# Kernel tuning notes

Hardware: AMD Instinct MI355X
Metric: run time of the kernel (lower is better)

## Reference

```python
import jax, jax.numpy as jnp
import numpy as np
import math

D_K = 1024
HEADS = 16
HEAD_DIM = 64

def setup_inputs() -> dict:
    key = jax.random.key(0)
    ks = jax.random.split(key, 9)
    B, S, E = 2, 2048, D_K
    sc = 0.02
    return {
        "x": jax.random.normal(ks[0], (B, S, E), dtype=jnp.float32),
        "mask": 1,
        "Wq": jax.random.normal(ks[1], (E, E), dtype=jnp.float32) * sc,
        "bq": jnp.zeros((E,), dtype=jnp.float32),
        "Wk": jax.random.normal(ks[2], (E, E), dtype=jnp.float32) * sc,
        "bk": jnp.zeros((E,), dtype=jnp.float32),
        "Wv": jax.random.normal(ks[3], (E, E), dtype=jnp.float32) * sc,
        "bv": jnp.zeros((E,), dtype=jnp.float32),
        "Wo": jax.random.normal(ks[4], (E, E), dtype=jnp.float32) * sc,
        "bo": jnp.zeros((E,), dtype=jnp.float32),
    }

def reference(x, mask, Wq, bq, Wk, bk, Wv, bv, Wo, bo):
    B, S, E = x.shape
    H, Dh = HEADS, HEAD_DIM
    # QKV projections; split heads: [B, H, S, Dh]
    q = (x @ Wq + bq).reshape(B, S, H, Dh).transpose(0, 2, 1, 3)
    k = (x @ Wk + bk).reshape(B, S, H, Dh).transpose(0, 2, 1, 3)
    v = (x @ Wv + bv).reshape(B, S, H, Dh).transpose(0, 2, 1, 3)
    # NOTE: original scales by sqrt(d_k) (full model dim), not sqrt(head_dim)
    scores = jnp.einsum('bhsd,bhtd->bhst', q, k) / math.sqrt(E)
    if mask:
        causal = jnp.tril(jnp.ones((S, S), dtype=bool))
        scores = jnp.where(causal[None, None], scores, jnp.float32(-1e9))
    attn = jax.nn.softmax(scores, axis=-1)
    out = jnp.einsum('bhst,bhtd->bhsd', attn, v)  # [B,H,S,Dh]
    out = out.transpose(0, 2, 1, 3).reshape(B, S, E)
    return out @ Wo + bo
```

## Files before the change

### kernel.cpp

```cpp
#include <hip/hip_runtime.h>

#define HEADS  16
#define DH     64
#define SEQ    2048
#define NBATCH 2
#define EMB    1024
#define MTOT   (NBATCH * SEQ)

#define QSCALE 0.045084220027780106f

typedef short  s16x8 __attribute__((ext_vector_type(8)));
typedef float  f32x4 __attribute__((ext_vector_type(4)));
typedef unsigned short u16;
typedef unsigned short u16x4 __attribute__((ext_vector_type(4)));

__device__ __forceinline__ u16 f2bf(float f) {
  unsigned u = __builtin_bit_cast(unsigned, f);
  u += 0x7fffu + ((u >> 16) & 1u);
  return (u16)(u >> 16);
}

__device__ __forceinline__ void gll16(const u16* g, u16* l) {
  __builtin_amdgcn_global_load_lds(
      (const __attribute__((address_space(1))) unsigned int*)g,
      (__attribute__((address_space(3))) unsigned int*)l, 16, 0, 0);
}

__global__ void cvt_x_kernel(const float* __restrict__ x, u16* __restrict__ xb) {
  int i = (blockIdx.x * 256 + threadIdx.x) * 4;
  float4 v = *(const float4*)(x + i);
  u16x4 o;
  o.x = f2bf(v.x); o.y = f2bf(v.y); o.z = f2bf(v.z); o.w = f2bf(v.w);
  *(u16x4*)(xb + i) = o;
}

__global__ __launch_bounds__(256) void cvt_wt_kernel(const float* __restrict__ Wq, const float* __restrict__ Wk,
                                                     const float* __restrict__ Wv, const float* __restrict__ Wo,
                                                     u16* __restrict__ Wqt, u16* __restrict__ Wkt,
                                                     u16* __restrict__ Wvt, u16* __restrict__ Wot) {
  __shared__ float tile[64][65];
  const float* W; u16* T;
  switch (blockIdx.z) {
    case 0:  W = Wq; T = Wqt; break;
    case 1:  W = Wk; T = Wkt; break;
    case 2:  W = Wv; T = Wvt; break;
    default: W = Wo; T = Wot; break;
  }
  const int n0 = blockIdx.x * 64, k0 = blockIdx.y * 64;
  const int tr = threadIdx.x >> 4;
  const int tc = (threadIdx.x & 15) * 4;
#pragma unroll
  for (int rr = 0; rr < 64; rr += 16) {
    float4 v = *(const float4*)&W[(size_t)(k0 + tr + rr) * EMB + n0 + tc];
    tile[tr + rr][tc + 0] = v.x;
    tile[tr + rr][tc + 1] = v.y;
    tile[tr + rr][tc + 2] = v.z;
    tile[tr + rr][tc + 3] = v.w;
  }
  __syncthreads();
#pragma unroll
  for (int rr = 0; rr < 64; rr += 16) {
    u16x4 o;
    o.x = f2bf(tile[tc + 0][tr + rr]);
    o.y = f2bf(tile[tc + 1][tr + rr]);
    o.z = f2bf(tile[tc + 2][tr + rr]);
    o.w = f2bf(tile[tc + 3][tr + rr]);
    *(u16x4*)&T[(size_t)(n0 + tr + rr) * EMB + k0 + tc] = o;
  }
}

__device__ __forceinline__ void gemm_core(const u16* __restrict__ A, const u16* __restrict__ Bt,
                                          u16* As, u16* Bs, int m0, int n0, f32x4 acc[4][2]) {
  const int tid = threadIdx.x;
  const int lane = tid & 63, w = tid >> 6;
  const int wm = w >> 1, wn = w & 1;
  const int lr = lane & 15, lq = lane >> 4;
#pragma unroll
  for (int i = 0; i < 4; i++)
#pragma unroll
    for (int j = 0; j < 2; j++)
      acc[i][j] = (f32x4){0.f, 0.f, 0.f, 0.f};

  for (int k0 = 0; k0 < EMB; k0 += 64) {
    __syncthreads();
#pragma unroll
    for (int j = 0; j < 4; j++) {
      int c = tid + 256 * j;
      int row = c >> 3, c8 = (c & 7) ^ (row & 7);
      gll16(&A[(size_t)(m0 + row) * EMB + k0 + c8 * 8],
            &As[(w * 64 + 256 * j) * 8]);
    }
#pragma unroll
    for (int j = 0; j < 2; j++) {
      int c = tid + 256 * j;
      int row = c >> 3, c8 = (c & 7) ^ (row & 7);
      gll16(&Bt[(size_t)(n0 + row) * EMB + k0 + c8 * 8],
            &Bs[(w * 64 + 256 * j) * 8]);
    }
    __syncthreads();
#pragma unroll
    for (int kk8 = 0; kk8 < 8; kk8 += 4) {
      s16x8 af[4], bf[2];
#pragma unroll
      for (int i = 0; i < 4; i++) {
        int row = wm * 64 + i * 16 + lr;
        af[i] = *(const s16x8*)&As[row * 64 + (((kk8 + lq) ^ (row & 7)) * 8)];
      }
#pragma unroll
      for (int j = 0; j < 2; j++) {
        int row = wn * 32 + j * 16 + lr;
        bf[j] = *(const s16x8*)&Bs[row * 64 + (((kk8 + lq) ^ (row & 7)) * 8)];
      }
#pragma unroll
      for (int i = 0; i < 4; i++)
#pragma unroll
        for (int j = 0; j < 2; j++)
          acc[i][j] = __builtin_amdgcn_mfma_f32_16x16x32_bf16(af[i], bf[j], acc[i][j], 0, 0, 0);
    }
  }
}

__global__ __launch_bounds__(256) void gemm_qkv(const u16* __restrict__ xb,
                                                const u16* __restrict__ Wqt, const u16* __restrict__ Wkt,
                                                const u16* __restrict__ Wvt,
                                                const float* __restrict__ bq, const float* __restrict__ bk,
                                                const float* __restrict__ bv,
                                                u16* __restrict__ Qb, u16* __restrict__ Kb,
                                                u16* __restrict__ Vtb) {
  __shared__ __align__(16) u16 As[128 * 64];
  __shared__ __align__(16) u16 Bs[64 * 64];
  const u16* Bt; const float* bias; u16* out; const int mode = blockIdx.z;
  switch (mode) {
    case 0:  Bt = Wqt; bias = bq; out = Qb;  break;
    case 1:  Bt = Wkt; bias = bk; out = Kb;  break;
    default: Bt = Wvt; bias = bv; out = Vtb; break;
  }
  const int m0 = blockIdx.y * 128, n0 = blockIdx.x * 64;
  f32x4 acc[4][2];
  gemm_core(xb, Bt, As, Bs, m0, n0, acc);

  const int tid = threadIdx.x, lane = tid & 63, w = tid >> 6;
  const int wm = w >> 1, wn = w & 1;
  const int lr = lane & 15, lq = lane >> 4;
#pragma unroll
  for (int i = 0; i < 4; i++) {
#pragma unroll
    for (int j = 0; j < 2; j++) {
      int col   = n0 + wn * 32 + j * 16 + lr;
      int mbase = m0 + wm * 64 + i * 16 + lq * 4;
      float bv_ = bias[col];
      int h = col >> 6, d = col & 63;
      if (mode == 0) {
#pragma unroll
        for (int r = 0; r < 4; r++) {
          int m = mbase + r, b = m >> 11, s = m & (SEQ - 1);
          out[((size_t)(b * HEADS + h) * SEQ + s) * DH + d] = f2bf((acc[i][j][r] + bv_) * QSCALE);
        }
      } else if (mode == 1) {
#pragma unroll
        for (int r = 0; r < 4; r++) {
          int m = mbase + r, b = m >> 11, s = m & (SEQ - 1);
          out[((size_t)(b * HEADS + h) * SEQ + s) * DH + d] = f2bf(acc[i][j][r] + bv_);
        }
      } else {
        int b = mbase >> 11, s = mbase & (SEQ - 1);
        u16x4 pk;
        pk.x = f2bf(acc[i][j][0] + bv_);
        pk.y = f2bf(acc[i][j][1] + bv_);
        pk.z = f2bf(acc[i][j][2] + bv_);
        pk.w = f2bf(acc[i][j][3] + bv_);
        *(u16x4*)&out[((size_t)(b * HEADS + h) * DH + d) * SEQ + s] = pk;
      }
    }
  }
}

__global__ __launch_bounds__(256) void gemm_out(const u16* __restrict__ A, const u16* __restrict__ Bt,
                                                const float* __restrict__ bias, float* __restrict__ out) {
  __shared__ __align__(16) u16 As[128 * 64];
  __shared__ __align__(16) u16 Bs[64 * 64];
  const int m0 = blockIdx.y * 128, n0 = blockIdx.x * 64;
  f32x4 acc[4][2];
  gemm_core(A, Bt, As, Bs, m0, n0, acc);

  const int tid = threadIdx.x, lane = tid & 63, w = tid >> 6;
  const int wm = w >> 1, wn = w & 1;
  const int lr = lane & 15, lq = lane >> 4;
#pragma unroll
  for (int i = 0; i < 4; i++) {
#pragma unroll
    for (int j = 0; j < 2; j++) {
      int col   = n0 + wn * 32 + j * 16 + lr;
      int mbase = m0 + wm * 64 + i * 16 + lq * 4;
      float bv_ = bias[col];
#pragma unroll
      for (int r = 0; r < 4; r++)
        out[(size_t)(mbase + r) * EMB + col] = acc[i][j][r] + bv_;
    }
  }
}

__global__ __launch_bounds__(512, 4) void attn_fwd(const u16* __restrict__ Q,
                                                   const u16* __restrict__ Kg,
                                                   const u16* __restrict__ Vt,
                                                   u16* __restrict__ O) {
  __shared__ __align__(16) u16 smem[33280];
  const int tid = threadIdx.x, lane = tid & 63, w = tid >> 6;
  const int g = w >> 2, wg = w & 3;
  const int lr = lane & 15, lq = lane >> 4;
  const int bh = blockIdx.y, bx = blockIdx.x;
  const int qtA = bx, qtB = 31 - bx;
  const int rowoff = wg * 16;
  u16* Ks = smem + (g ? 11520 : 0);
  u16* Vs = smem + (g ? 16640 : 5120);
  u16* pw = smem + 23040 + w * 1280;
  const size_t qkbase = (size_t)bh * SEQ * DH;
  const size_t vbase  = (size_t)bh * DH * SEQ;
  const u16* kgp = Kg + qkbase;
  const u16* vtp = Vt + vbase;
  const int t256 = tid & 255;
  const int b = bh >> 4, hh = bh & 15;

  {
    int r = t256 >> 4, c = (t256 & 15) * 4;
    u16 one = 0x3F80;
    u16x4 val = (r == 0) ? (u16x4){one, one, one, one} : (u16x4){0, 0, 0, 0};
    *(u16x4*)&Vs[(64 + r) * 80 + c] = val;
  }

  s16x8 qf0, qf1;
  {
    const int myqt0 = g ? qtB : qtA;
    const u16* qp = Q + qkbase + (size_t)(myqt0 * 64 + rowoff + lr) * DH;
    qf0 = *(const s16x8*)&qp[lq * 8];
    qf1 = *(const s16x8*)&qp[32 + lq * 8];
  }
  f32x4 o[4], os;
#pragma unroll
  for (int t = 0; t < 4; t++) o[t] = (f32x4){0.f, 0.f, 0.f, 0.f};
  os = (f32x4){0.f, 0.f, 0.f, 0.f};

  const int srow = t256 >> 3, soff = (t256 & 7) * 8;
  int kt0 = g ? (16 - bx) : 0;
  s16x8 kr0 = *(const s16x8*)&kgp[(size_t)(kt0 * 64 + srow) * DH + soff];
  s16x8 kr1 = *(const s16x8*)&kgp[(size_t)(kt0 * 64 + srow + 32) * DH + soff];
  s16x8 vr0 = *(const s16x8*)&vtp[(size_t)srow * SEQ + kt0 * 64 + soff];
  s16x8 vr1 = *(const s16x8*)&vtp[(size_t)(srow + 32) * SEQ + kt0 * 64 + soff];

  for (int i = 0; i < 17; ++i) {
    __syncthreads();
    *(s16x8*)&Ks[srow * 80 + soff]        = kr0;
    *(s16x8*)&Ks[(srow + 32) * 80 + soff] = kr1;
    *(s16x8*)&Vs[srow * 80 + soff]        = vr0;
    *(s16x8*)&Vs[(srow + 32) * 80 + soff] = vr1;
    __syncthreads();

    {
      bool hn = g ? (i + 1 < 16) : (i + 1 < 17);
      if (hn) {
        int ktn = g ? (17 + i - bx) : ((i + 1 <= qtA) ? (i + 1) : (i - qtA));
        kr0 = *(const s16x8*)&kgp[(size_t)(ktn * 64 + srow) * DH + soff];
        kr1 = *(const s16x8*)&kgp[(size_t)(ktn * 64 + srow + 32) * DH + soff];
        vr0 = *(const s16x8*)&vtp[(size_t)srow * SEQ + ktn * 64 + soff];
        vr1 = *(const s16x8*)&vtp[(size_t)(srow + 32) * SEQ + ktn * 64 + soff];
      }
    }

    if (g == 0 && i == qtA + 1) {
      float inv[4];
#pragma unroll
      for (int r = 0; r < 4; r++) inv[r] = __builtin_amdgcn_rcpf(__shfl(os[r], lq * 16));
#pragma unroll
      for (int t = 0; t < 4; t++)
#pragma unroll
        for (int r = 0; r < 4; r++) {
          int m = b * SEQ + qtA * 64 + rowoff + lq * 4 + r;
          O[(size_t)m * EMB + hh * 64 + t * 16 + lr] = f2bf(o[t][r] * inv[r]);
        }
#pragma unroll
      for (int t = 0; t < 4; t++) o[t] = (f32x4){0.f, 0.f, 0.f, 0.f};
      os = (f32x4){0.f, 0.f, 0.f, 0.f};
      const u16* qp = Q + qkbase + (size_t)(qtB * 64 + rowoff + lr) * DH;
      qf0 = *(const s16x8*)&qp[lq * 8];
      qf1 = *(const s16x8*)&qp[32 + lq * 8];
    }

    const bool docomp = g ? (i < 16) : true;
    if (docomp) {
      f32x4 sc[4];
#pragma unroll
      for (int t = 0; t < 4; t++) {
        s16x8 kf0 = *(const s16x8*)&Ks[(t * 16 + lr) * 80 + lq * 8];
        s16x8 kf1 = *(const s16x8*)&Ks[(t * 16 + lr) * 80 + 32 + lq * 8];
        f32x4 z = (f32x4){0.f, 0.f, 0.f, 0.f};
        z = __builtin_amdgcn_mfma_f32_16x16x32_bf16(kf0, qf0, z, 0, 0, 0);
        z = __builtin_amdgcn_mfma_f32_16x16x32_bf16(kf1, qf1, z, 0, 0, 0);
        sc[t] = z;
      }
      const bool diag = g ? (i == 15) : (i == qtA);
      if (diag) {
#pragma unroll
        for (int t = 0; t < 4; t++)
#pragma unroll
          for (int r = 0; r < 4; r++)
            if ((t * 16 + lq * 4 + r) > (rowoff + lr)) sc[t][r] = -1e9f;
      }
#pragma unroll
      for (int t = 0; t < 4; t++)
#pragma unroll
        for (int r = 0; r < 4; r++)
          sc[t][r] = __builtin_amdgcn_exp2f(sc[t][r]);

#pragma unroll
      for (int t = 0; t < 4; t++) {
        u16x4 pk;
        pk.x = f2bf(sc[t][0]);
        pk.y = f2bf(sc[t][1]);
        pk.z = f2bf(sc[t][2]);
        pk.w = f2bf(sc[t][3]);
        *(u16x4*)&pw[lr * 80 + t * 16 + lq * 4] = pk;
      }

#pragma unroll
      for (int kc = 0; kc < 2; kc++) {
        s16x8 pf = *(const s16x8*)&pw[lr * 80 + kc * 32 + lq * 8];
#pragma unroll
        for (int t = 0; t < 4; t++) {
          s16x8 vf = *(const s16x8*)&Vs[(t * 16 + lr) * 80 + kc * 32 + lq * 8];
          o[t] = __builtin_amdgcn_mfma_f32_16x16x32_bf16(pf, vf, o[t], 0, 0, 0);
        }
        s16x8 sf = *(const s16x8*)&Vs[(64 + lr) * 80 + kc * 32 + lq * 8];
        os = __builtin_amdgcn_mfma_f32_16x16x32_bf16(pf, sf, os, 0, 0, 0);
      }
    }
  }

  __syncthreads();
  float* Cb = (float*)smem;
  float* Ss = (float*)(smem + 23040);
  if (g == 0) {
#pragma unroll
    for (int t = 0; t < 4; t++)
#pragma unroll
      for (int r = 0; r < 4; r++)
        Cb[(rowoff + lq * 4 + r) * 68 + t * 16 + lr] = o[t][r];
#pragma unroll
    for (int r = 0; r < 4; r++) {
      float s = __shfl(os[r], lq * 16);
      if (lr == 0) Ss[rowoff + lq * 4 + r] = s;
    }
  }
  __syncthreads();
  if (g == 1) {
    float inv[4];
#pragma unroll
    for (int r = 0; r < 4; r++)
      inv[r] = __builtin_amdgcn_rcpf(__shfl(os[r], lq * 16) + Ss[rowoff + lq * 4 + r]);
#pragma unroll
    for (int t = 0; t < 4; t++)
#pragma unroll
      for (int r = 0; r < 4; r++) {
        int m = b * SEQ + qtB * 64 + rowoff + lq * 4 + r;
        float v = o[t][r] + Cb[(rowoff + lq * 4 + r) * 68 + t * 16 + lr];
        O[(size_t)m * EMB + hh * 64 + t * 16 + lr] = f2bf(v * inv[r]);
      }
  }
}

extern "C" void kernel_launch(void* const* d_in, const int* in_sizes, int n_in,
                              void* d_out, int out_size, void* d_ws, size_t ws_size,
                              hipStream_t stream) {
  const float* x  = (const float*)d_in[0];
  const float* Wq = (const float*)d_in[2];
  const float* bq = (const float*)d_in[3];
  const float* Wk = (const float*)d_in[4];
  const float* bk = (const float*)d_in[5];
  const float* Wv = (const float*)d_in[6];
  const float* bv = (const float*)d_in[7];
  const float* Wo = (const float*)d_in[8];
  const float* bo = (const float*)d_in[9];

  char* ws = (char*)d_ws;
  const size_t MB = 1024 * 1024;
  u16* Qb  = (u16*)(ws + 0 * MB);
  u16* Kb  = (u16*)(ws + 8 * MB);
  u16* Vtb = (u16*)(ws + 16 * MB);
  u16* xb  = (u16*)(ws + 24 * MB);
  u16* Ob  = xb;
  u16* Wqt = (u16*)(ws + 32 * MB);
  u16* Wkt = (u16*)(ws + 34 * MB);
  u16* Wvt = (u16*)(ws + 36 * MB);
  u16* Wot = (u16*)(ws + 38 * MB);

  cvt_x_kernel<<<(MTOT * EMB) / (256 * 4), 256, 0, stream>>>(x, xb);
  cvt_wt_kernel<<<dim3(EMB / 64, EMB / 64, 4), 256, 0, stream>>>(
      Wq, Wk, Wv, Wo, Wqt, Wkt, Wvt, Wot);

  gemm_qkv<<<dim3(EMB / 64, MTOT / 128, 3), 256, 0, stream>>>(
      xb, Wqt, Wkt, Wvt, bq, bk, bv, Qb, Kb, Vtb);

  attn_fwd<<<dim3(16, NBATCH * HEADS), 512, 0, stream>>>(Qb, Kb, Vtb, Ob);

  gemm_out<<<dim3(EMB / 64, MTOT / 128), 256, 0, stream>>>(Ob, Wot, bo, (float*)d_out);
}
```

Measured before the change: 189.3 us.

## Halve attention block to 256 threads with two query row-tiles per wave

The attention kernel now runs 4 waves per block instead of 8, and each wave computes two 16-row query sub-tiles that share the K and V fragments loaded from LDS. Each thread stages both halves' K/V tiles into shared memory. The aim is to amortize LDS fragment reads over more MFMA work and cut per-block thread overhead. The cost is more registers per wave, from doubled accumulators and prefetch buffers, and fewer waves to hide latency with 512 blocks.

```diff
diff --git a/kernel.cpp b/kernel.cpp
--- a/kernel.cpp
+++ b/kernel.cpp
@@ -200,137 +200,182 @@
   }
 }
 
-__global__ __launch_bounds__(512, 4) void attn_fwd(const u16* __restrict__ Q,
-                                                   const u16* __restrict__ Kg,
-                                                   const u16* __restrict__ Vt,
-                                                   u16* __restrict__ O) {
+__global__ __launch_bounds__(256) void attn_fwd(const u16* __restrict__ Q,
+                                                const u16* __restrict__ Kg,
+                                                const u16* __restrict__ Vt,
+                                                u16* __restrict__ O) {
   __shared__ __align__(16) u16 smem[33280];
   const int tid = threadIdx.x, lane = tid & 63, w = tid >> 6;
-  const int g = w >> 2, wg = w & 3;
+  const int g = w >> 1, wg = w & 1;
   const int lr = lane & 15, lq = lane >> 4;
   const int bh = blockIdx.y, bx = blockIdx.x;
   const int qtA = bx, qtB = 31 - bx;
-  const int rowoff = wg * 16;
+  const int ro0 = wg * 32, ro1 = wg * 32 + 16;
   u16* Ks = smem + (g ? 11520 : 0);
   u16* Vs = smem + (g ? 16640 : 5120);
-  u16* pw = smem + 23040 + w * 1280;
+  u16* KsA = smem;           u16* VsA = smem + 5120;
+  u16* KsB = smem + 11520;   u16* VsB = smem + 16640;
+  u16* pw0 = smem + 23040 + (w * 2 + 0) * 1280;
+  u16* pw1 = smem + 23040 + (w * 2 + 1) * 1280;
   const size_t qkbase = (size_t)bh * SEQ * DH;
   const size_t vbase  = (size_t)bh * DH * SEQ;
   const u16* kgp = Kg + qkbase;
   const u16* vtp = Vt + vbase;
-  const int t256 = tid & 255;
   const int b = bh >> 4, hh = bh & 15;
 
   {
-    int r = t256 >> 4, c = (t256 & 15) * 4;
+    int r = tid >> 4, c = (tid & 15) * 4;
     u16 one = 0x3F80;
     u16x4 val = (r == 0) ? (u16x4){one, one, one, one} : (u16x4){0, 0, 0, 0};
-    *(u16x4*)&Vs[(64 + r) * 80 + c] = val;
-  }
-
-  s16x8 qf0, qf1;
+    *(u16x4*)&VsA[(64 + r) * 80 + c] = val;
+    *(u16x4*)&VsB[(64 + r) * 80 + c] = val;
+  }
+
+  s16x8 qa0, qa1, qb0, qb1;
   {
     const int myqt0 = g ? qtB : qtA;
-    const u16* qp = Q + qkbase + (size_t)(myqt0 * 64 + rowoff + lr) * DH;
-    qf0 = *(const s16x8*)&qp[lq * 8];
-    qf1 = *(const s16x8*)&qp[32 + lq * 8];
-  }
-  f32x4 o[4], os;
-#pragma unroll
-  for (int t = 0; t < 4; t++) o[t] = (f32x4){0.f, 0.f, 0.f, 0.f};
-  os = (f32x4){0.f, 0.f, 0.f, 0.f};
-
-  const int srow = t256 >> 3, soff = (t256 & 7) * 8;
-  int kt0 = g ? (16 - bx) : 0;
-  s16x8 kr0 = *(const s16x8*)&kgp[(size_t)(kt0 * 64 + srow) * DH + soff];
-  s16x8 kr1 = *(const s16x8*)&kgp[(size_t)(kt0 * 64 + srow + 32) * DH + soff];
-  s16x8 vr0 = *(const s16x8*)&vtp[(size_t)srow * SEQ + kt0 * 64 + soff];
-  s16x8 vr1 = *(const s16x8*)&vtp[(size_t)(srow + 32) * SEQ + kt0 * 64 + soff];
+    const u16* qp0 = Q + qkbase + (size_t)(myqt0 * 64 + ro0 + lr) * DH;
+    const u16* qp1 = Q + qkbase + (size_t)(myqt0 * 64 + ro1 + lr) * DH;
+    qa0 = *(const s16x8*)&qp0[lq * 8];
+    qa1 = *(const s16x8*)&qp0[32 + lq * 8];
+    qb0 = *(const s16x8*)&qp1[lq * 8];
+    qb1 = *(const s16x8*)&qp1[32 + lq * 8];
+  }
+  f32x4 o0[4], o1[4], os0, os1;
+#pragma unroll
+  for (int t = 0; t < 4; t++) { o0[t] = (f32x4){0.f,0.f,0.f,0.f}; o1[t] = (f32x4){0.f,0.f,0.f,0.f}; }
+  os0 = (f32x4){0.f,0.f,0.f,0.f};
+  os1 = (f32x4){0.f,0.f,0.f,0.f};
+
+  const int srow = tid >> 3, soff = (tid & 7) * 8;
+  int ktA = 0, ktB = 16 - bx;
+  s16x8 kA0 = *(const s16x8*)&kgp[(size_t)(ktA * 64 + srow) * DH + soff];
+  s16x8 kA1 = *(const s16x8*)&kgp[(size_t)(ktA * 64 + srow + 32) * DH + soff];
+  s16x8 vA0 = *(const s16x8*)&vtp[(size_t)srow * SEQ + ktA * 64 + soff];
+  s16x8 vA1 = *(const s16x8*)&vtp[(size_t)(srow + 32) * SEQ + ktA * 64 + soff];
+  s16x8 kB0 = *(const s16x8*)&kgp[(size_t)(ktB * 64 + srow) * DH + soff];
+  s16x8 kB1 = *(const s16x8*)&kgp[(size_t)(ktB * 64 + srow + 32) * DH + soff];
+  s16x8 vB0 = *(const s16x8*)&vtp[(size_t)srow * SEQ + ktB * 64 + soff];
+  s16x8 vB1 = *(const s16x8*)&vtp[(size_t)(srow + 32) * SEQ + ktB * 64 + soff];
 
   for (int i = 0; i < 17; ++i) {
     __syncthreads();
-    *(s16x8*)&Ks[srow * 80 + soff]        = kr0;
-    *(s16x8*)&Ks[(srow + 32) * 80 + soff] = kr1;
-    *(s16x8*)&Vs[srow * 80 + soff]        = vr0;
-    *(s16x8*)&Vs[(srow + 32) * 80 + soff] = vr1;
+    *(s16x8*)&KsA[srow * 80 + soff]        = kA0;
+    *(s16x8*)&KsA[(srow + 32) * 80 + soff] = kA1;
+    *(s16x8*)&VsA[srow * 80 + soff]        = vA0;
+    *(s16x8*)&VsA[(srow + 32) * 80 + soff] = vA1;
+    *(s16x8*)&KsB[srow * 80 + soff]        = kB0;
+    *(s16x8*)&KsB[(srow + 32) * 80 + soff] = kB1;
+    *(s16x8*)&VsB[srow * 80 + soff]        = vB0;
+    *(s16x8*)&VsB[(srow + 32) * 80 + soff] = vB1;
     __syncthreads();
 
-    {
-      bool hn = g ? (i + 1 < 16) : (i + 1 < 17);
-      if (hn) {
-        int ktn = g ? (17 + i - bx) : ((i + 1 <= qtA) ? (i + 1) : (i - qtA));
-        kr0 = *(const s16x8*)&kgp[(size_t)(ktn * 64 + srow) * DH + soff];
-        kr1 = *(const s16x8*)&kgp[(size_t)(ktn * 64 + srow + 32) * DH + soff];
-        vr0 = *(const s16x8*)&vtp[(size_t)srow * SEQ + ktn * 64 + soff];
-        vr1 = *(const s16x8*)&vtp[(size_t)(srow + 32) * SEQ + ktn * 64 + soff];
-      }
+    if (i + 1 < 17) {
+      int ktnA = (i + 1 <= qtA) ? (i + 1) : (i - qtA);
+      kA0 = *(const s16x8*)&kgp[(size_t)(ktnA * 64 + srow) * DH + soff];
+      kA1 = *(const s16x8*)&kgp[(size_t)(ktnA * 64 + srow + 32) * DH + soff];
+      vA0 = *(const s16x8*)&vtp[(size_t)srow * SEQ + ktnA * 64 + soff];
+      vA1 = *(const s16x8*)&vtp[(size_t)(srow + 32) * SEQ + ktnA * 64 + soff];
+    }
+    if (i + 1 < 16) {
+      int ktnB = 17 + i - bx;
+      kB0 = *(const s16x8*)&kgp[(size_t)(ktnB * 64 + srow) * DH + soff];
+      kB1 = *(const s16x8*)&kgp[(size_t)(ktnB * 64 + srow + 32) * DH + soff];
+      vB0 = *(const s16x8*)&vtp[(size_t)srow * SEQ + ktnB * 64 + soff];
+      vB1 = *(const s16x8*)&vtp[(size_t)(srow + 32) * SEQ + ktnB * 64 + soff];
     }
 
     if (g == 0 && i == qtA + 1) {
       float inv[4];
 #pragma unroll
-      for (int r = 0; r < 4; r++) inv[r] = __builtin_amdgcn_rcpf(__shfl(os[r], lq * 16));
+      for (int r = 0; r < 4; r++) inv[r] = __builtin_amdgcn_rcpf(__shfl(os0[r], lq * 16));
 #pragma unroll
       for (int t = 0; t < 4; t++)
 #pragma unroll
         for (int r = 0; r < 4; r++) {
-          int m = b * SEQ + qtA * 64 + rowoff + lq * 4 + r;
-          O[(size_t)m * EMB + hh * 64 + t * 16 + lr] = f2bf(o[t][r] * inv[r]);
-        }
-#pragma unroll
-      for (int t = 0; t < 4; t++) o[t] = (f32x4){0.f, 0.f, 0.f, 0.f};
-      os = (f32x4){0.f, 0.f, 0.f, 0.f};
-      const u16* qp = Q + qkbase + (size_t)(qtB * 64 + rowoff + lr) * DH;
-      qf0 = *(const s16x8*)&qp[lq * 8];
-      qf1 = *(const s16x8*)&qp[32 + lq * 8];
+          int m = b * SEQ + qtA * 64 + ro0 + lq * 4 + r;
+          O[(size_t)m * EMB + hh * 64 + t * 16 + lr] = f2bf(o0[t][r] * inv[r]);
+        }
+#pragma unroll
+      for (int r = 0; r < 4; r++) inv[r] = __builtin_amdgcn_rcpf(__shfl(os1[r], lq * 16));
+#pragma unroll
+      for (int t = 0; t < 4; t++)
+#pragma unroll
+        for (int r = 0; r < 4; r++) {
+          int m = b * SEQ + qtA * 64 + ro1 + lq * 4 + r;
+          O[(size_t)m * EMB + hh * 64 + t * 16 + lr] = f2bf(o1[t][r] * inv[r]);
+        }
+#pragma unroll
+      for (int t = 0; t < 4; t++) { o0[t] = (f32x4){0.f,0.f,0.f,0.f}; o1[t] = (f32x4){0.f,0.f,0.f,0.f}; }
+      os0 = (f32x4){0.f,0.f,0.f,0.f};
+      os1 = (f32x4){0.f,0.f,0.f,0.f};
+      const u16* qp0 = Q + qkbase + (size_t)(qtB * 64 + ro0 + lr) * DH;
+      const u16* qp1 = Q + qkbase + (size_t)(qtB * 64 + ro1 + lr) * DH;
+      qa0 = *(const s16x8*)&qp0[lq * 8];
+      qa1 = *(const s16x8*)&qp0[32 + lq * 8];
+      qb0 = *(const s16x8*)&qp1[lq * 8];
+      qb1 = *(const s16x8*)&qp1[32 + lq * 8];
     }
 
     const bool docomp = g ? (i < 16) : true;
     if (docomp) {
-      f32x4 sc[4];
+      f32x4 sc0[4], sc1[4];
 #pragma unroll
       for (int t = 0; t < 4; t++) {
         s16x8 kf0 = *(const s16x8*)&Ks[(t * 16 + lr) * 80 + lq * 8];
         s16x8 kf1 = *(const s16x8*)&Ks[(t * 16 + lr) * 80 + 32 + lq * 8];
-        f32x4 z = (f32x4){0.f, 0.f, 0.f, 0.f};
-        z = __builtin_amdgcn_mfma_f32_16x16x32_bf16(kf0, qf0, z, 0, 0, 0);
-        z = __builtin_amdgcn_mfma_f32_16x16x32_bf16(kf1, qf1, z, 0, 0, 0);
-        sc[t] = z;
+        f32x4 z0 = (f32x4){0.f, 0.f, 0.f, 0.f};
+        z0 = __builtin_amdgcn_mfma_f32_16x16x32_bf16(kf0, qa0, z0, 0, 0, 0);
+        z0 = __builtin_amdgcn_mfma_f32_16x16x32_bf16(kf1, qa1, z0, 0, 0, 0);
+        sc0[t] = z0;
+        f32x4 z1 = (f32x4){0.f, 0.f, 0.f, 0.f};
+        z1 = __builtin_amdgcn_mfma_f32_16x16x32_bf16(kf0, qb0, z1, 0, 0, 0);
+        z1 = __builtin_amdgcn_mfma_f32_16x16x32_bf16(kf1, qb1, z1, 0, 0, 0);
+        sc1[t] = z1;
       }
       const bool diag = g ? (i == 15) : (i == qtA);
       if (diag) {
 #pragma unroll
         for (int t = 0; t < 4; t++)
 #pragma unroll
-          for (int r = 0; r < 4; r++)
-            if ((t * 16 + lq * 4 + r) > (rowoff + lr)) sc[t][r] = -1e9f;
+          for (int r = 0; r < 4; r++) {
+            int key = t * 16 + lq * 4 + r;
+            if (key > (ro0 + lr)) sc0[t][r] = -1e9f;
+            if (key > (ro1 + lr)) sc1[t][r] = -1e9f;
+          }
       }
 #pragma unroll
       for (int t = 0; t < 4; t++)
 #pragma unroll
-        for (int r = 0; r < 4; r++)
-          sc[t][r] = __builtin_amdgcn_exp2f(sc[t][r]);
+        for (int r = 0; r < 4; r++) {
+          sc0[t][r] = __builtin_amdgcn_exp2f(sc0[t][r]);
+          sc1[t][r] = __builtin_amdgcn_exp2f(sc1[t][r]);
+        }
 
 #pragma unroll
       for (int t = 0; t < 4; t++) {
-        u16x4 pk;
-        pk.x = f2bf(sc[t][0]);
-        pk.y = f2bf(sc[t][1]);
-        pk.z = f2bf(sc[t][2]);
-        pk.w = f2bf(sc[t][3]);
-        *(u16x4*)&pw[lr * 80 + t * 16 + lq * 4] = pk;
+        u16x4 p0, p1;
+        p0.x = f2bf(sc0[t][0]); p0.y = f2bf(sc0[t][1]);
+        p0.z = f2bf(sc0[t][2]); p0.w = f2bf(sc0[t][3]);
+        *(u16x4*)&pw0[lr * 80 + t * 16 + lq * 4] = p0;
+        p1.x = f2bf(sc1[t][0]); p1.y = f2bf(sc1[t][1]);
+        p1.z = f2bf(sc1[t][2]); p1.w = f2bf(sc1[t][3]);
+        *(u16x4*)&pw1[lr * 80 + t * 16 + lq * 4] = p1;
       }
 
 #pragma unroll
       for (int kc = 0; kc < 2; kc++) {
-        s16x8 pf = *(const s16x8*)&pw[lr * 80 + kc * 32 + lq * 8];
+        s16x8 pf0 = *(const s16x8*)&pw0[lr * 80 + kc * 32 + lq * 8];
+        s16x8 pf1 = *(const s16x8*)&pw1[lr * 80 + kc * 32 + lq * 8];
 #pragma unroll
         for (int t = 0; t < 4; t++) {
           s16x8 vf = *(const s16x8*)&Vs[(t * 16 + lr) * 80 + kc * 32 + lq * 8];
-          o[t] = __builtin_amdgcn_mfma_f32_16x16x32_bf16(pf, vf, o[t], 0, 0, 0);
+          o0[t] = __builtin_amdgcn_mfma_f32_16x16x32_bf16(pf0, vf, o0[t], 0, 0, 0);
+          o1[t] = __builtin_amdgcn_mfma_f32_16x16x32_bf16(pf1, vf, o1[t], 0, 0, 0);
         }
         s16x8 sf = *(const s16x8*)&Vs[(64 + lr) * 80 + kc * 32 + lq * 8];
-        os = __builtin_amdgcn_mfma_f32_16x16x32_bf16(pf, sf, os, 0, 0, 0);
+        os0 = __builtin_amdgcn_mfma_f32_16x16x32_bf16(pf0, sf, os0, 0, 0, 0);
+        os1 = __builtin_amdgcn_mfma_f32_16x16x32_bf16(pf1, sf, os1, 0, 0, 0);
       }
     }
   }
@@ -342,12 +387,18 @@
 #pragma unroll
     for (int t = 0; t < 4; t++)
 #pragma unroll
-      for (int r = 0; r < 4; r++)
-        Cb[(rowoff + lq * 4 + r) * 68 + t * 16 + lr] = o[t][r];
+      for (int r = 0; r < 4; r++) {
+        Cb[(ro0 + lq * 4 + r) * 68 + t * 16 + lr] = o0[t][r];
+        Cb[(ro1 + lq * 4 + r) * 68 + t * 16 + lr] = o1[t][r];
+      }
 #pragma unroll
     for (int r = 0; r < 4; r++) {
-      float s = __shfl(os[r], lq * 16);
-      if (lr == 0) Ss[rowoff + lq * 4 + r] = s;
+      float s0 = __shfl(os0[r], lq * 16);
+      float s1 = __shfl(os1[r], lq * 16);
+      if (lr == 0) {
+        Ss[ro0 + lq * 4 + r] = s0;
+        Ss[ro1 + lq * 4 + r] = s1;
+      }
     }
   }
   __syncthreads();
@@ -355,13 +406,24 @@
     float inv[4];
 #pragma unroll
     for (int r = 0; r < 4; r++)
-      inv[r] = __builtin_amdgcn_rcpf(__shfl(os[r], lq * 16) + Ss[rowoff + lq * 4 + r]);
+      inv[r] = __builtin_amdgcn_rcpf(__shfl(os0[r], lq * 16) + Ss[ro0 + lq * 4 + r]);
 #pragma unroll
     for (int t = 0; t < 4; t++)
 #pragma unroll
       for (int r = 0; r < 4; r++) {
-        int m = b * SEQ + qtB * 64 + rowoff + lq * 4 + r;
-        float v = o[t][r] + Cb[(rowoff + lq * 4 + r) * 68 + t * 16 + lr];
+        int m = b * SEQ + qtB * 64 + ro0 + lq * 4 + r;
+        float v = o0[t][r] + Cb[(ro0 + lq * 4 + r) * 68 + t * 16 + lr];
+        O[(size_t)m * EMB + hh * 64 + t * 16 + lr] = f2bf(v * inv[r]);
+      }
+#pragma unroll
+    for (int r = 0; r < 4; r++)
+      inv[r] = __builtin_amdgcn_rcpf(__shfl(os1[r], lq * 16) + Ss[ro1 + lq * 4 + r]);
+#pragma unroll
+    for (int t = 0; t < 4; t++)
+#pragma unroll
+      for (int r = 0; r < 4; r++) {
+        int m = b * SEQ + qtB * 64 + ro1 + lq * 4 + r;
+        float v = o1[t][r] + Cb[(ro1 + lq * 4 + r) * 68 + t * 16 + lr];
         O[(size_t)m * EMB + hh * 64 + t * 16 + lr] = f2bf(v * inv[r]);
       }
   }
@@ -399,7 +461,7 @@
   gemm_qkv<<<dim3(EMB / 64, MTOT / 128, 3), 256, 0, stream>>>(
       xb, Wqt, Wkt, Wvt, bq, bk, bv, Qb, Kb, Vtb);
 
-  attn_fwd<<<dim3(16, NBATCH * HEADS), 512, 0, stream>>>(Qb, Kb, Vtb, Ob);
+  attn_fwd<<<dim3(16, NBATCH * HEADS), 256, 0, stream>>>(Qb, Kb, Vtb, Ob);
 
   gemm_out<<<dim3(EMB / 64, MTOT / 128), 256, 0, stream>>>(Ob, Wot, bo, (float*)d_out);
 }
```

After: 193.2 us. 2.1% more time.
